# Performance work log

Hardware: AMD Instinct MI355X
Metric: run time of the kernel (lower is better)

## Reference

```python
import jax, jax.numpy as jnp
import numpy as np
import math

D, H = 128, 8
B, LC, LQ = 8, 512, 64


def pos_signal(channels, length):
    # tensor2tensor timing signal, returned as [C, L]
    pos = jnp.arange(length, dtype=jnp.float32)
    nts = channels // 2
    inc = math.log(1.0e4) / (nts - 1)
    inv = jnp.exp(jnp.arange(nts, dtype=jnp.float32) * -inc)
    st = pos[:, None] * inv[None, :]                      # [L, nts]
    sig = jnp.concatenate([jnp.sin(st), jnp.cos(st)], 1)  # [L, C]
    return sig.T


def mask_logits(t, m):
    return t * m + (1.0 - m) * -1e30


def ln_c(x, g, b):  # LayerNorm over channel dim of [B, D, L]
    mu = jnp.mean(x, axis=1, keepdims=True)
    var = jnp.mean((x - mu) ** 2, axis=1, keepdims=True)
    return (x - mu) / jnp.sqrt(var + 1e-5) * g[None, :, None] + b[None, :, None]


def conv1x1(x, w, b=None):  # x [B, I, L], w [O, I]
    y = jnp.einsum('oi,bil->bol', w, x)
    return y if b is None else y + b[None, :, None]


def dw_sep_conv(x, dw, pw, pwb):  # depthwise (k, no bias) -> pointwise (bias) -> relu
    k = dw.shape[-1]
    y = jax.lax.conv_general_dilated(x, dw[:, None, :], (1,), [(k // 2, k // 2)],
        dimension_numbers=('NCH', 'OIH', 'NCH'), feature_group_count=x.shape[1])
    return jax.nn.relu(conv1x1(y, pw, pwb))


def self_attention(x, mem_w, q_w, mask, n_head):  # x [B, D, L]
    b, d, L = x.shape
    dh = d // n_head
    mem = jnp.einsum('oi,bil->blo', mem_w, x)  # [B, L, 2D]
    q = jnp.einsum('oi,bil->blo', q_w, x)      # [B, L, D]
    def heads(t):
        return t.reshape(b, L, n_head, dh).transpose(0, 2, 1, 3)  # [B, H, L, dh]
    Qh = heads(q) * dh ** -0.5
    K = heads(mem[..., :d])
    V = heads(mem[..., d:])
    logits = jnp.einsum('bhqe,bhke->bhqk', Qh, K)
    logits = mask_logits(logits, mask[:, None, None, :])
    w = jax.nn.softmax(logits, axis=-1)
    o = jnp.einsum('bhqk,bhke->bhqe', w, V)
    return o.transpose(0, 2, 1, 3).reshape(b, L, d).transpose(0, 2, 1)


def encoder_block(x, mask, p, n_head):
    out = x + pos_signal(x.shape[1], x.shape[2])[None]
    n_conv = p['dw'].shape[0]
    for i in range(n_conv):
        res = out
        out = ln_c(out, p['lnc_g'][i], p['lnc_b'][i])
        out = dw_sep_conv(out, p['dw'][i], p['pw'][i], p['pw_b'][i]) + res
    res = out
    out = ln_c(out, p['ln1_g'], p['ln1_b'])
    out = self_attention(out, p['mem_w'], p['q_w'], mask, n_head) + res
    res = out
    out = ln_c(out, p['ln2_g'], p['ln2_b'])
    out = jax.nn.relu(conv1x1(out, p['ffn1_w'], p['ffn1_b']))
    out = conv1x1(out, p['ffn2_w'], p['ffn2_b'])
    return out + res


def cq_attention(Ce, Qe, cmask, qmask, w4C, w4Q, w4mlu, cq_b):
    Cx = Ce.transpose(0, 2, 1)   # [B, Lc, 2D]
    Qx = Qe.transpose(0, 2, 1)   # [B, Lq, 2D]
    s0 = jnp.einsum('bld,d->bl', Cx, w4C)[:, :, None]
    s1 = jnp.einsum('bqd,d->bq', Qx, w4Q)[:, None, :]
    s2 = jnp.einsum('bld,bqd->blq', Cx * w4mlu[None, None, :], Qx)
    S = s0 + s1 + s2 + cq_b
    S1 = jax.nn.softmax(mask_logits(S, qmask[:, None, :]), axis=2)
    S2 = jax.nn.softmax(mask_logits(S, cmask[:, :, None]), axis=1)
    A = jnp.einsum('blq,bqd->bld', S1, Qx)
    Bt = jnp.einsum('blq,bmq,bmd->bld', S1, S2, Cx)  # (S1 @ S2^T) @ C
    out = jnp.concatenate([Cx, A, Cx * A, Cx * Bt], axis=2)
    return out.transpose(0, 2, 1)  # [B, 8D, Lc]


def _forward(C, Q, maskC, maskQ, e_dw, e_pw, e_pw_b, e_lnc_g, e_lnc_b, e_mem_w, e_q_w,
             e_ffn1_w, e_ffn1_b, e_ffn2_w, e_ffn2_b, e_ln1_g, e_ln1_b, e_ln2_g, e_ln2_b,
             w4C, w4Q, w4mlu, cq_b, resizer_w,
             m_dw, m_pw, m_pw_b, m_lnc_g, m_lnc_b, m_mem_w, m_q_w,
             m_ffn1_w, m_ffn1_b, m_ffn2_w, m_ffn2_b, m_ln1_g, m_ln1_b, m_ln2_g, m_ln2_b):
    ep = dict(dw=e_dw, pw=e_pw, pw_b=e_pw_b, lnc_g=e_lnc_g, lnc_b=e_lnc_b,
              mem_w=e_mem_w, q_w=e_q_w, ffn1_w=e_ffn1_w, ffn1_b=e_ffn1_b,
              ffn2_w=e_ffn2_w, ffn2_b=e_ffn2_b, ln1_g=e_ln1_g, ln1_b=e_ln1_b,
              ln2_g=e_ln2_g, ln2_b=e_ln2_b)
    mp = dict(dw=m_dw, pw=m_pw, pw_b=m_pw_b, lnc_g=m_lnc_g, lnc_b=m_lnc_b,
              mem_w=m_mem_w, q_w=m_q_w, ffn1_w=m_ffn1_w, ffn1_b=m_ffn1_b,
              ffn2_w=m_ffn2_w, ffn2_b=m_ffn2_b, ln1_g=m_ln1_g, ln1_b=m_ln1_b,
              ln2_g=m_ln2_g, ln2_b=m_ln2_b)
    Ce = encoder_block(C, maskC, ep, H)
    Qe = encoder_block(Q, maskQ, ep, H)
    Ce = jnp.concatenate([Ce, C], axis=1)  # encode_fusion -> [B, 2D, Lc]
    Qe = jnp.concatenate([Qe, Q], axis=1)
    X = cq_attention(Ce, Qe, maskC, maskQ, w4C, w4Q, w4mlu, cq_b)
    X = jnp.concatenate([X, Ce], axis=1)   # match_fusion -> [B, 10D, Lc]
    M0 = conv1x1(X, resizer_w)             # [B, D, Lc]

    def run(m):
        def step(carry, p):
            return encoder_block(carry, maskC, p, H), None
        m, _ = jax.lax.scan(step, m, mp)
        return m

    M1 = run(M0)
    M2 = run(M1)
    M3 = run(M2)
    return M1, M2, M3


def setup_inputs() -> dict:
    key = jax.random.key(0)
    ks = iter(jax.random.split(key, 48))
    def rn(shape, scale):
        return jax.random.normal(next(ks), shape, dtype=jnp.float32) * scale
    s1 = 1.0 / math.sqrt(D)
    s2 = 1.0 / math.sqrt(2 * D)
    f32 = jnp.float32
    return dict(
        C=rn((B, D, LC), 1.0), Q=rn((B, D, LQ), 1.0),
        maskC=jnp.ones((B, LC), f32), maskQ=jnp.ones((B, LQ), f32),
        e_dw=rn((4, D, 7), 1.0 / math.sqrt(7)), e_pw=rn((4, D, D), s1),
        e_pw_b=jnp.zeros((4, D), f32), e_lnc_g=jnp.ones((4, D), f32), e_lnc_b=jnp.zeros((4, D), f32),
        e_mem_w=rn((2 * D, D), s1), e_q_w=rn((D, D), s1),
        e_ffn1_w=rn((D, D), s1), e_ffn1_b=jnp.zeros((D,), f32),
        e_ffn2_w=rn((D, D), s1), e_ffn2_b=jnp.zeros((D,), f32),
        e_ln1_g=jnp.ones((D,), f32), e_ln1_b=jnp.zeros((D,), f32),
        e_ln2_g=jnp.ones((D,), f32), e_ln2_b=jnp.zeros((D,), f32),
        w4C=rn((2 * D,), s2), w4Q=rn((2 * D,), s2), w4mlu=rn((2 * D,), s2),
        cq_b=jnp.zeros((1,), f32),
        resizer_w=rn((D, 10 * D), 1.0 / math.sqrt(10 * D)),
        m_dw=rn((7, 2, D, 5), 1.0 / math.sqrt(5)), m_pw=rn((7, 2, D, D), s1),
        m_pw_b=jnp.zeros((7, 2, D), f32), m_lnc_g=jnp.ones((7, 2, D), f32), m_lnc_b=jnp.zeros((7, 2, D), f32),
        m_mem_w=rn((7, 2 * D, D), s1), m_q_w=rn((7, D, D), s1),
        m_ffn1_w=rn((7, D, D), s1), m_ffn1_b=jnp.zeros((7, D), f32),
        m_ffn2_w=rn((7, D, D), s1), m_ffn2_b=jnp.zeros((7, D), f32),
        m_ln1_g=jnp.ones((7, D), f32), m_ln1_b=jnp.zeros((7, D), f32),
        m_ln2_g=jnp.ones((7, D), f32), m_ln2_b=jnp.zeros((7, D), f32),
    )


def reference(C, Q, maskC, maskQ, e_dw, e_pw, e_pw_b, e_lnc_g, e_lnc_b, e_mem_w, e_q_w,
              e_ffn1_w, e_ffn1_b, e_ffn2_w, e_ffn2_b, e_ln1_g, e_ln1_b, e_ln2_g, e_ln2_b,
              w4C, w4Q, w4mlu, cq_b, resizer_w,
              m_dw, m_pw, m_pw_b, m_lnc_g, m_lnc_b, m_mem_w, m_q_w,
              m_ffn1_w, m_ffn1_b, m_ffn2_w, m_ffn2_b, m_ln1_g, m_ln1_b, m_ln2_g, m_ln2_b):
    return _forward(C, Q, maskC, maskQ, e_dw, e_pw, e_pw_b, e_lnc_g, e_lnc_b, e_mem_w, e_q_w,
                    e_ffn1_w, e_ffn1_b, e_ffn2_w, e_ffn2_b, e_ln1_g, e_ln1_b, e_ln2_g, e_ln2_b,
                    w4C, w4Q, w4mlu, cq_b, resizer_w,
                    m_dw, m_pw, m_pw_b, m_lnc_g, m_lnc_b, m_mem_w, m_q_w,
                    m_ffn1_w, m_ffn1_b, m_ffn2_w, m_ffn2_b, m_ln1_g, m_ln1_b, m_ln2_g, m_ln2_b)
```

## Files before the change

kernel.cpp:

```cpp
#include <hip/hip_runtime.h>
#include <math.h>

#define D_  128
#define B_  8
#define H_  8
#define LC_ 512
#define LQ_ 64

typedef float f32x4 __attribute__((ext_vector_type(4)));
typedef short bf16x8 __attribute__((ext_vector_type(8)));
typedef short short4v __attribute__((ext_vector_type(4)));
typedef unsigned short ushortT;

__device__ inline short bfr(float x) {
  unsigned u = __float_as_uint(x);
  u += 0x7fff + ((u >> 16) & 1);
  return (short)(u >> 16);
}
__device__ inline float bfi(ushortT u) {
  return __uint_as_float(((unsigned)u) << 16);
}

__device__ inline bf16x8 mk8(short4v lo, short4v hi) {
  bf16x8 r;
  r[0] = lo[0]; r[1] = lo[1]; r[2] = lo[2]; r[3] = lo[3];
  r[4] = hi[0]; r[5] = hi[1]; r[6] = hi[2]; r[7] = hi[3];
  return r;
}

__device__ inline bf16x8 ldA(const ushortT* row, int koff) {
  short4v lo = *(const short4v*)(row + koff);
  short4v hi = *(const short4v*)(row + koff + 16);
  return mk8(lo, hi);
}
__device__ inline bf16x8 ldB2(const ushortT* plo, const ushortT* phi) {
  short4v lo = *(const short4v*)plo;
  short4v hi = *(const short4v*)phi;
  return mk8(lo, hi);
}

__global__ void k_prep(const float* a0, const float* a1, const float* a2,
                       const float* a3, const float* a4, const float* a5,
                       const float* a6, const float* a7, const float* a8,
                       const float* a9, const float* a10, ushortT* dst) {
  int i = blockIdx.x * 256 + threadIdx.x;
  if (i >= 1114112) return;
  const float* s; int lo;
  if      (i <   65536) { s = a0;  lo = i; }
  else if (i <   98304) { s = a1;  lo = i - 65536; }
  else if (i <  114688) { s = a2;  lo = i - 98304; }
  else if (i <  131072) { s = a3;  lo = i - 114688; }
  else if (i <  147456) { s = a4;  lo = i - 131072; }
  else if (i <  311296) { s = a5;  lo = i - 147456; }
  else if (i <  540672) { s = a6;  lo = i - 311296; }
  else if (i <  770048) { s = a7;  lo = i - 540672; }
  else if (i <  884736) { s = a8;  lo = i - 770048; }
  else if (i <  999424) { s = a9;  lo = i - 884736; }
  else                  { s = a10; lo = i - 999424; }
  dst[i] = (ushortT)bfr(s[lo]);
}

__global__ void k_postab(float* pos) {
  int i = blockIdx.x * 256 + threadIdx.x;
  int d = i >> 9, l = i & 511;
  int j = d & 63;
  float arg = (float)l * expf(-(float)j * 0.14619588f);
  pos[i] = (d < 64) ? sinf(arg) : cosf(arg);
}

template <int KK, int ADDPOS>
__global__ __launch_bounds__(256) void k_fusedconv(
    const float* __restrict__ xC, float* __restrict__ yC,
    const float* __restrict__ xQ, float* __restrict__ yQ,
    const float* __restrict__ pos,
    const float* __restrict__ dw1, const ushortT* __restrict__ pw1,
    const float* __restrict__ pb1, const float* __restrict__ g1,
    const float* __restrict__ be1,
    const float* __restrict__ dw2, const ushortT* __restrict__ pw2,
    const float* __restrict__ pb2, const float* __restrict__ g2w,
    const float* __restrict__ be2, int ntC) {
  const int HALO = KK / 2;
  const int W1 = 32 + 2 * HALO;
  __shared__ __align__(16) float raw[128 * 40];
  __shared__ __align__(16) ushortT l1o[128 * 36];
  __shared__ __align__(16) ushortT xbf1[32 * 32 * 4];
  __shared__ float mu1[40], rs1[40], mu2[32], rs2[32], ps[160], psq[160];
  ushortT* xbf2 = (ushortT*)raw;
  int bx = blockIdx.x;
  const float* x; float* yout; int l0, L;
  if (bx < ntC) { x = xC; yout = yC; l0 = bx * 16; L = LC_; }
  else          { x = xQ; yout = yQ; l0 = (bx - ntC) * 16; L = LQ_; }
  int o0 = blockIdx.y * 64;
  int b = blockIdx.z;
  int tid = threadIdx.x;
  for (int idx = tid; idx < 128 * W1; idx += 256) {
    int d = idx / W1, c = idx - d * W1;
    int gl = l0 - 8 - HALO + c;
    float v = 0.f;
    if (gl >= 0 && gl < L) {
      v = x[((size_t)b * 128 + d) * L + gl];
      if (ADDPOS) v += pos[d * 512 + gl];
    }
    raw[d * 40 + c] = v;
  }
  __syncthreads();
  if (tid < 4 * W1) {
    int c = tid % W1, hh = tid / W1;
    float s = 0.f, s2 = 0.f;
    for (int d = hh * 32; d < hh * 32 + 32; d++) {
      float v = raw[d * 40 + c];
      s += v; s2 += v * v;
    }
    ps[tid] = s; psq[tid] = s2;
  }
  __syncthreads();
  if (tid < W1) {
    float s = ps[tid] + ps[tid + W1] + ps[tid + 2 * W1] + ps[tid + 3 * W1];
    float s2 = psq[tid] + psq[tid + W1] + psq[tid + 2 * W1] + psq[tid + 3 * W1];
    float mu = s * (1.f / 128.f);
    float var = fmaxf(s2 * (1.f / 128.f) - mu * mu, 0.f);
    mu1[tid] = mu; rs1[tid] = rsqrtf(var + 1e-5f);
  }
  __syncthreads();
  {
    int cc0 = tid & 31, dbase = tid >> 5;
#pragma unroll
    for (int kq = 0; kq < 4; kq++) {
      short4v pk;
#pragma unroll
      for (int e = 0; e < 4; e++) {
        int d = dbase * 16 + kq * 4 + e;
        float gg = g1[d], bb = be1[d];
        const float* wr = dw1 + d * KK;
        float acc = 0.f;
#pragma unroll
        for (int t = 0; t < KK; t++) {
          int ci = cc0 + t;
          int gl = l0 - 8 - HALO + ci;
          float lv = 0.f;
          if (gl >= 0 && gl < L)
            lv = (raw[d * 40 + ci] - mu1[ci]) * rs1[ci] * gg + bb;
          acc += wr[t] * lv;
        }
        pk[e] = bfr(acc);
      }
      *(short4v*)&xbf1[(((dbase * 4 + kq) * 32) + cc0) * 4] = pk;
    }
  }
  __syncthreads();
  int w = tid >> 6, lane = tid & 63, g2 = lane >> 4, r = lane & 15;
  {
    f32x4 acc[2][2];
#pragma unroll
    for (int i = 0; i < 2; i++)
#pragma unroll
      for (int nt = 0; nt < 2; nt++) acc[i][nt] = (f32x4){0.f, 0.f, 0.f, 0.f};
#pragma unroll
    for (int i = 0; i < 2; i++) {
      const ushortT* arow = pw1 + (size_t)((2 * w + i) * 16 + r) * 128;
#pragma unroll
      for (int kk = 0; kk < 4; kk++) {
        bf16x8 a = ldA(arow, kk * 32 + g2 * 4);
#pragma unroll
        for (int nt = 0; nt < 2; nt++) {
          bf16x8 bb = ldB2(&xbf1[(((kk * 8 + g2) * 32) + nt * 16 + r) * 4],
                           &xbf1[(((kk * 8 + 4 + g2) * 32) + nt * 16 + r) * 4]);
          acc[i][nt] = __builtin_amdgcn_mfma_f32_16x16x32_bf16(a, bb, acc[i][nt], 0, 0, 0);
        }
      }
    }
#pragma unroll
    for (int i = 0; i < 2; i++)
#pragma unroll
      for (int nt = 0; nt < 2; nt++)
#pragma unroll
        for (int p = 0; p < 4; p++) {
          int o = (2 * w + i) * 16 + g2 * 4 + p;
          int c1 = nt * 16 + r;
          int gl = l0 - 8 + c1;
          float val = 0.f;
          if (gl >= 0 && gl < L)
            val = fmaxf(acc[i][nt][p] + pb1[o], 0.f) + raw[o * 40 + c1 + HALO];
          l1o[o * 36 + c1] = (ushortT)bfr(val);
        }
  }
  __syncthreads();
  if (tid < 128) {
    int c = tid & 31, hh = tid >> 5;
    float s = 0.f, s2 = 0.f;
    for (int d = hh * 32; d < hh * 32 + 32; d++) {
      float v = bfi(l1o[d * 36 + c]);
      s += v; s2 += v * v;
    }
    ps[tid] = s; psq[tid] = s2;
  }
  __syncthreads();
  if (tid < 32) {
    float s = ps[tid] + ps[tid + 32] + ps[tid + 64] + ps[tid + 96];
    float s2 = psq[tid] + psq[tid + 32] + psq[tid + 64] + psq[tid + 96];
    float mu = s * (1.f / 128.f);
    float var = fmaxf(s2 * (1.f / 128.f) - mu * mu, 0.f);
    mu2[tid] = mu; rs2[tid] = rsqrtf(var + 1e-5f);
  }
  __syncthreads();
  {
    int cc2 = tid & 15, db2 = tid >> 4;
#pragma unroll
    for (int kq = 0; kq < 2; kq++) {
      short4v pk;
#pragma unroll
      for (int e = 0; e < 4; e++) {
        int d = db2 * 8 + kq * 4 + e;
        float gg = g2w[d], bb = be2[d];
        const float* wr = dw2 + d * KK;
        float acc = 0.f;
#pragma unroll
        for (int t = 0; t < KK; t++) {
          int c1 = cc2 + 8 + t - HALO;
          int gl = l0 + cc2 + t - HALO;
          float lv = 0.f;
          if (gl >= 0 && gl < L)
            lv = (bfi(l1o[d * 36 + c1]) - mu2[c1]) * rs2[c1] * gg + bb;
          acc += wr[t] * lv;
        }
        pk[e] = bfr(acc);
      }
      *(short4v*)&xbf2[(((db2 * 2 + kq) * 16) + cc2) * 4] = pk;
    }
  }
  __syncthreads();
  {
    f32x4 a2 = {0.f, 0.f, 0.f, 0.f};
    const ushortT* arow = pw2 + (size_t)(o0 + 16 * w + r) * 128;
#pragma unroll
    for (int kk = 0; kk < 4; kk++) {
      bf16x8 a = ldA(arow, kk * 32 + g2 * 4);
      bf16x8 bb = ldB2(&xbf2[(((kk * 8 + g2) * 16) + r) * 4],
                       &xbf2[(((kk * 8 + 4 + g2) * 16) + r) * 4]);
      a2 = __builtin_amdgcn_mfma_f32_16x16x32_bf16(a, bb, a2, 0, 0, 0);
    }
#pragma unroll
    for (int p = 0; p < 4; p++) {
      int o = o0 + 16 * w + g2 * 4 + p;
      yout[((size_t)b * 128 + o) * L + l0 + r] =
          fmaxf(a2[p] + pb2[o], 0.f) + bfi(l1o[o * 36 + 8 + r]);
    }
  }
}

template <int KK, int ADDPOS>
__global__ __launch_bounds__(1024) void k_convproj1024(
    const float* __restrict__ xC, float* __restrict__ yC,
    ushortT* __restrict__ mkvC, ushortT* __restrict__ qpC,
    const float* __restrict__ xQ, float* __restrict__ yQ,
    ushortT* __restrict__ mkvQ, ushortT* __restrict__ qpQ,
    const float* __restrict__ pos,
    const float* __restrict__ dw1, const ushortT* __restrict__ pw1,
    const float* __restrict__ pb1, const float* __restrict__ g1,
    const float* __restrict__ be1,
    const float* __restrict__ dw2, const ushortT* __restrict__ pw2,
    const float* __restrict__ pb2, const float* __restrict__ g2w,
    const float* __restrict__ be2,
    const ushortT* __restrict__ memw, const ushortT* __restrict__ qw,
    const float* __restrict__ g3, const float* __restrict__ be3, int ntC) {
  const int HALO = KK / 2;
  const int W1 = 32 + 2 * HALO;
  __shared__ __align__(16) float raw[128 * 40];
  __shared__ __align__(16) ushortT l1o[128 * 36];
  __shared__ __align__(16) ushortT xbf1[32 * 32 * 4];
  __shared__ __align__(16) ushortT c2o[128 * 16];
  __shared__ float mu1[40], rs1[40], mu2[32], rs2[32], mu3[16], rs3[16];
  __shared__ float ps[160], psq[160];
  ushortT* xbf2 = (ushortT*)raw;
  ushortT* xbf3 = (ushortT*)(raw + 4096);
  int bx = blockIdx.x;
  const float* x; float* yout; ushortT* mkv; ushortT* qp; int l0, L;
  if (bx < ntC) { x = xC; yout = yC; mkv = mkvC; qp = qpC; l0 = bx * 16; L = LC_; }
  else          { x = xQ; yout = yQ; mkv = mkvQ; qp = qpQ; l0 = (bx - ntC) * 16; L = LQ_; }
  int b = blockIdx.z;
  int tid = threadIdx.x;
  for (int idx = tid; idx < 128 * W1; idx += 1024) {
    int d = idx / W1, c = idx - d * W1;
    int gl = l0 - 8 - HALO + c;
    float v = 0.f;
    if (gl >= 0 && gl < L) {
      v = x[((size_t)b * 128 + d) * L + gl];
      if (ADDPOS) v += pos[d * 512 + gl];
    }
    raw[d * 40 + c] = v;
  }
  __syncthreads();
  if (tid < 4 * W1) {
    int c = tid % W1, hh = tid / W1;
    float s = 0.f, s2 = 0.f;
    for (int d = hh * 32; d < hh * 32 + 32; d++) {
      float v = raw[d * 40 + c];
      s += v; s2 += v * v;
    }
    ps[tid] = s; psq[tid] = s2;
  }
  __syncthreads();
  if (tid < W1) {
    float s = ps[tid] + ps[tid + W1] + ps[tid + 2 * W1] + ps[tid + 3 * W1];
    float s2 = psq[tid] + psq[tid + W1] + psq[tid + 2 * W1] + psq[tid + 3 * W1];
    float mu = s * (1.f / 128.f);
    float var = fmaxf(s2 * (1.f / 128.f) - mu * mu, 0.f);
    mu1[tid] = mu; rs1[tid] = rsqrtf(var + 1e-5f);
  }
  __syncthreads();
  {
    int cc0 = tid & 31, dbase = tid >> 5;
    short4v pk;
#pragma unroll
    for (int e = 0; e < 4; e++) {
      int d = dbase * 4 + e;
      float gg = g1[d], bb = be1[d];
      const float* wr = dw1 + d * KK;
      float acc = 0.f;
#pragma unroll
      for (int t = 0; t < KK; t++) {
        int ci = cc0 + t;
        int gl = l0 - 8 - HALO + ci;
        float lv = 0.f;
        if (gl >= 0 && gl < L)
          lv = (raw[d * 40 + ci] - mu1[ci]) * rs1[ci] * gg + bb;
        acc += wr[t] * lv;
      }
      pk[e] = bfr(acc);
    }
    *(short4v*)&xbf1[((dbase * 32) + cc0) * 4] = pk;
  }
  __syncthreads();
  int w = tid >> 6, lane = tid & 63, g2 = lane >> 4, r = lane & 15;
  {
    int m = w & 7, nt = w >> 3;
    f32x4 acc = {0.f, 0.f, 0.f, 0.f};
    const ushortT* arow = pw1 + (size_t)(m * 16 + r) * 128;
#pragma unroll
    for (int kk = 0; kk < 4; kk++) {
      bf16x8 a = ldA(arow, kk * 32 + g2 * 4);
      bf16x8 bb = ldB2(&xbf1[(((kk * 8 + g2) * 32) + nt * 16 + r) * 4],
                       &xbf1[(((kk * 8 + 4 + g2) * 32) + nt * 16 + r) * 4]);
      acc = __builtin_amdgcn_mfma_f32_16x16x32_bf16(a, bb, acc, 0, 0, 0);
    }
#pragma unroll
    for (int p = 0; p < 4; p++) {
      int o = m * 16 + g2 * 4 + p;
      int c1 = nt * 16 + r;
      int gl = l0 - 8 + c1;
      float val = 0.f;
      if (gl >= 0 && gl < L)
        val = fmaxf(acc[p] + pb1[o], 0.f) + raw[o * 40 + c1 + HALO];
      l1o[o * 36 + c1] = (ushortT)bfr(val);
    }
  }
  __syncthreads();
  if (tid < 128) {
    int c = tid & 31, hh = tid >> 5;
    float s = 0.f, s2 = 0.f;
    for (int d = hh * 32; d < hh * 32 + 32; d++) {
      float v = bfi(l1o[d * 36 + c]);
      s += v; s2 += v * v;
    }
    ps[tid] = s; psq[tid] = s2;
  }
  __syncthreads();
  if (tid < 32) {
    float s = ps[tid] + ps[tid + 32] + ps[tid + 64] + ps[tid + 96];
    float s2 = psq[tid] + psq[tid + 32] + psq[tid + 64] + psq[tid + 96];
    float mu = s * (1.f / 128.f);
    float var = fmaxf(s2 * (1.f / 128.f) - mu * mu, 0.f);
    mu2[tid] = mu; rs2[tid] = rsqrtf(var + 1e-5f);
  }
  __syncthreads();
  {
    int cc2 = tid & 15, db2 = tid >> 4;
#pragma unroll
    for (int e = 0; e < 2; e++) {
      int d = db2 * 2 + e;
      float gg = g2w[d], bb = be2[d];
      const float* wr = dw2 + d * KK;
      float acc = 0.f;
#pragma unroll
      for (int t = 0; t < KK; t++) {
        int c1 = cc2 + 8 + t - HALO;
        int gl = l0 + cc2 + t - HALO;
        float lv = 0.f;
        if (gl >= 0 && gl < L)
          lv = (bfi(l1o[d * 36 + c1]) - mu2[c1]) * rs2[c1] * gg + bb;
        acc += wr[t] * lv;
      }
      xbf2[(((d >> 2) * 16) + cc2) * 4 + (d & 3)] = (ushortT)bfr(acc);
    }
  }
  __syncthreads();
  if (w < 8) {
    f32x4 a2 = {0.f, 0.f, 0.f, 0.f};
    const ushortT* arow = pw2 + (size_t)(w * 16 + r) * 128;
#pragma unroll
    for (int kk = 0; kk < 4; kk++) {
      bf16x8 a = ldA(arow, kk * 32 + g2 * 4);
      bf16x8 bb = ldB2(&xbf2[(((kk * 8 + g2) * 16) + r) * 4],
                       &xbf2[(((kk * 8 + 4 + g2) * 16) + r) * 4]);
      a2 = __builtin_amdgcn_mfma_f32_16x16x32_bf16(a, bb, a2, 0, 0, 0);
    }
#pragma unroll
    for (int p = 0; p < 4; p++) {
      int o = w * 16 + g2 * 4 + p;
      float val = fmaxf(a2[p] + pb2[o], 0.f) + bfi(l1o[o * 36 + 8 + r]);
      yout[((size_t)b * 128 + o) * L + l0 + r] = val;
      c2o[o * 16 + r] = (ushortT)bfr(val);
    }
  }
  __syncthreads();
  if (tid < 128) {
    int c = tid & 15, hh = tid >> 4;
    float s = 0.f, s2 = 0.f;
    for (int d = hh * 16; d < hh * 16 + 16; d++) {
      float v = bfi(c2o[d * 16 + c]);
      s += v; s2 += v * v;
    }
    ps[tid] = s; psq[tid] = s2;
  }
  __syncthreads();
  if (tid < 16) {
    float s = 0.f, s2 = 0.f;
#pragma unroll
    for (int hh = 0; hh < 8; hh++) { s += ps[hh * 16 + tid]; s2 += psq[hh * 16 + tid]; }
    float mu = s * (1.f / 128.f);
    float var = fmaxf(s2 * (1.f / 128.f) - mu * mu, 0.f);
    mu3[tid] = mu; rs3[tid] = rsqrtf(var + 1e-5f);
  }
  __syncthreads();
  for (int idx = tid; idx < 2048; idx += 1024) {
    int d = idx >> 4, c = idx & 15;
    float val = (bfi(c2o[d * 16 + c]) - mu3[c]) * rs3[c] * g3[d] + be3[d];
    xbf3[(((d >> 2) * 16) + c) * 4 + (d & 3)] = (ushortT)bfr(val);
  }
  __syncthreads();
#pragma unroll
  for (int t = 0; t < 2; t++) {
    int mt = w + 16 * t;
    if (mt < 24) {
      const ushortT* arow; ushortT* outp; int obase, O;
      if (mt < 16) { arow = memw + (size_t)(mt * 16 + r) * 128; outp = mkv; obase = mt * 16; O = 256; }
      else         { arow = qw + (size_t)((mt - 16) * 16 + r) * 128; outp = qp; obase = (mt - 16) * 16; O = 128; }
      f32x4 acc = {0.f, 0.f, 0.f, 0.f};
#pragma unroll
      for (int kk = 0; kk < 4; kk++) {
        bf16x8 a = ldA(arow, kk * 32 + g2 * 4);
        bf16x8 bb = ldB2(&xbf3[(((kk * 8 + g2) * 16) + r) * 4],
                         &xbf3[(((kk * 8 + 4 + g2) * 16) + r) * 4]);
        acc = __builtin_amdgcn_mfma_f32_16x16x32_bf16(a, bb, acc, 0, 0, 0);
      }
#pragma unroll
      for (int p = 0; p < 4; p++)
        outp[((size_t)b * O + obase + g2 * 4 + p) * L + l0 + r] = (ushortT)bfr(acc[p]);
    }
  }
}

template <int NCH, int WOUT>
__device__ __forceinline__ void attn_body(
    char* smem, const ushortT* memKV, const ushortT* qp, const float* mask,
    float* cur, const ushortT* w1bf, const float* b1,
    const ushortT* w2bf, const float* b2,
    const float* g, const float* be, float* wout, int q0, int b, int L, int tid) {
  float* msh = (float*)smem;
  float* ssh = (float*)(smem + 2048);
  float* OshF = (float*)(smem + 4096);
  float* updT = (float*)(smem + 12288);
  ushortT* xbf = (ushortT*)(smem + 20480);
  ushortT* midbf = (ushortT*)(smem + 24576);
  float* mu_s = (float*)(smem + 28672);
  float* rs_s = (float*)(smem + 28736);
  float* ps = (float*)(smem + 28800);
  float* psq = (float*)(smem + 32896);
  int w = tid >> 6;
  int h = w & 7, kh = w >> 3;
  int lane = tid & 63;
  int g2 = lane >> 4, r = lane & 15;
  const ushortT* qb = qp + ((size_t)b * 128 + h * 16) * L;
  const ushortT* kb = memKV + ((size_t)b * 256 + h * 16) * L;
  const ushortT* vb = memKV + ((size_t)b * 256 + 128 + h * 16) * L;
  const float* mk = mask + (size_t)b * L;
  int qcol = q0 + r;
  bf16x8 qf;
#pragma unroll
  for (int j = 0; j < 4; j++)
    qf[j] = bfr(bfi(qb[(size_t)(g2 * 4 + j) * L + qcol]) * 0.25f);
  qf[4] = 0; qf[5] = 0; qf[6] = 0; qf[7] = 0;
  float m_run = -INFINITY, ssum = 0.f;
  f32x4 O = {0.f, 0.f, 0.f, 0.f};
  int kbeg = kh * (L / 2), kend = (kh + 1) * (L / 2);
  for (int k0 = kbeg; k0 < kend; k0 += NCH * 16) {
    f32x4 sd[NCH];
#pragma unroll
    for (int mc = 0; mc < NCH; mc++) {
      bf16x8 kf;
      int krow = k0 + mc * 16 + r;
#pragma unroll
      for (int j = 0; j < 4; j++)
        kf[j] = (short)kb[(size_t)(g2 * 4 + j) * L + krow];
      kf[4] = 0; kf[5] = 0; kf[6] = 0; kf[7] = 0;
      f32x4 z = {0.f, 0.f, 0.f, 0.f};
      sd[mc] = __builtin_amdgcn_mfma_f32_16x16x32_bf16(kf, qf, z, 0, 0, 0);
    }
    float tm = -INFINITY;
#pragma unroll
    for (int mc = 0; mc < NCH; mc++) {
#pragma unroll
      for (int p = 0; p < 4; p++) {
        float mv = mk[k0 + mc * 16 + g2 * 4 + p];
        float sv = sd[mc][p] * mv + (1.f - mv) * (-1e30f);
        sd[mc][p] = sv;
        tm = fmaxf(tm, sv);
      }
    }
    tm = fmaxf(tm, __shfl_xor(tm, 16));
    tm = fmaxf(tm, __shfl_xor(tm, 32));
    float nm = fmaxf(m_run, tm);
    float c = __expf(m_run - nm);
    ssum *= c;
    O[0] *= c; O[1] *= c; O[2] *= c; O[3] *= c;
    float psum = 0.f;
    bf16x8 pf[NCH / 2];
#pragma unroll
    for (int c2 = 0; c2 < NCH / 2; c2++) {
#pragma unroll
      for (int j = 0; j < 4; j++) {
        float e0 = __expf(sd[2 * c2][j] - nm);
        float e1 = __expf(sd[2 * c2 + 1][j] - nm);
        psum += e0 + e1;
        pf[c2][j] = bfr(e0);
        pf[c2][j + 4] = bfr(e1);
      }
    }
    psum += __shfl_xor(psum, 16);
    psum += __shfl_xor(psum, 32);
    ssum += psum;
#pragma unroll
    for (int c2 = 0; c2 < NCH / 2; c2++) {
      const ushortT* vrow = vb + (size_t)r * L + k0 + c2 * 32 + g2 * 4;
      short4v lo = *(const short4v*)vrow;
      short4v hi = *(const short4v*)(vrow + 16);
      bf16x8 vf = mk8(lo, hi);
      O = __builtin_amdgcn_mfma_f32_16x16x32_bf16(vf, pf[c2], O, 0, 0, 0);
    }
    m_run = nm;
  }
  if (kh == 1) {
    msh[h * 64 + lane] = m_run;
    ssh[h * 64 + lane] = ssum;
#pragma unroll
    for (int p = 0; p < 4; p++) OshF[(h * 64 + lane) * 4 + p] = O[p];
  }
  __syncthreads();
  if (kh == 0) {
    float mB = msh[h * 64 + lane], sB = ssh[h * 64 + lane];
    float nm = fmaxf(m_run, mB);
    float cA = __expf(m_run - nm), cB = __expf(mB - nm);
    float inv = 1.f / (ssum * cA + sB * cB);
#pragma unroll
    for (int p = 0; p < 4; p++) {
      int d = h * 16 + g2 * 4 + p;
      float ov = (O[p] * cA + OshF[(h * 64 + lane) * 4 + p] * cB) * inv;
      updT[d * 16 + r] = cur[((size_t)b * 128 + d) * L + qcol] + ov;
    }
  }
  __syncthreads();
  {
    int c = tid & 15, hh = tid >> 4;
    float s = 0.f, s2 = 0.f;
    for (int d = hh * 2; d < hh * 2 + 2; d++) {
      float v = updT[d * 16 + c];
      s += v; s2 += v * v;
    }
    ps[tid] = s; psq[tid] = s2;
  }
  __syncthreads();
  if (tid < 16) {
    float s = 0.f, s2 = 0.f;
    for (int hh = 0; hh < 64; hh++) { s += ps[hh * 16 + tid]; s2 += psq[hh * 16 + tid]; }
    float mu = s * (1.f / 128.f);
    float var = fmaxf(s2 * (1.f / 128.f) - mu * mu, 0.f);
    mu_s[tid] = mu; rs_s[tid] = rsqrtf(var + 1e-5f);
  }
  __syncthreads();
  for (int idx = tid; idx < 2048; idx += 1024) {
    int d = idx >> 4, c = idx & 15;
    float val = (updT[d * 16 + c] - mu_s[c]) * rs_s[c] * g[d] + be[d];
    xbf[(((d >> 2) * 16) + c) * 4 + (d & 3)] = (ushortT)bfr(val);
  }
  __syncthreads();
  int w8 = tid >> 6;
  int g2b = (tid & 63) >> 4, rb = tid & 15;
  if (w8 < 8) {
    f32x4 acc = {0.f, 0.f, 0.f, 0.f};
    const ushortT* ar = w1bf + (size_t)(16 * w8 + rb) * 128;
#pragma unroll
    for (int kk = 0; kk < 4; kk++) {
      bf16x8 a = ldA(ar, kk * 32 + g2b * 4);
      bf16x8 bb = ldB2(&xbf[(((kk * 8 + g2b) * 16) + rb) * 4],
                       &xbf[(((kk * 8 + 4 + g2b) * 16) + rb) * 4]);
      acc = __builtin_amdgcn_mfma_f32_16x16x32_bf16(a, bb, acc, 0, 0, 0);
    }
#pragma unroll
    for (int p = 0; p < 4; p++) {
      int dmid = 16 * w8 + g2b * 4 + p;
      float val = fmaxf(acc[p] + b1[dmid], 0.f);
      midbf[(((4 * w8 + g2b) * 16) + rb) * 4 + p] = (ushortT)bfr(val);
    }
  }
  __syncthreads();
  if (w8 < 8) {
    f32x4 a2 = {0.f, 0.f, 0.f, 0.f};
    const ushortT* ar = w2bf + (size_t)(16 * w8 + rb) * 128;
#pragma unroll
    for (int kk = 0; kk < 4; kk++) {
      bf16x8 a = ldA(ar, kk * 32 + g2b * 4);
      bf16x8 bb = ldB2(&midbf[(((kk * 8 + g2b) * 16) + rb) * 4],
                       &midbf[(((kk * 8 + 4 + g2b) * 16) + rb) * 4]);
      a2 = __builtin_amdgcn_mfma_f32_16x16x32_bf16(a, bb, a2, 0, 0, 0);
    }
#pragma unroll
    for (int p = 0; p < 4; p++) {
      int o = 16 * w8 + g2b * 4 + p;
      size_t pos2 = ((size_t)b * 128 + o) * L + q0 + rb;
      float val = a2[p] + b2[o] + updT[o * 16 + rb];
      cur[pos2] = val;
      if (WOUT) wout[pos2] = val;
    }
  }
}

template <int WOUT>
__global__ __launch_bounds__(1024) void k_attnffn_m(
    const ushortT* memKV, const ushortT* qp, const float* mask, float* cur,
    const ushortT* w1bf, const float* b1, const ushortT* w2bf, const float* b2,
    const float* g, const float* be, float* wout) {
  __shared__ __align__(16) char smem[36992];
  attn_body<8, WOUT>(smem, memKV, qp, mask, cur, w1bf, b1, w2bf, b2, g, be,
                     wout, blockIdx.x * 16, blockIdx.z, LC_, threadIdx.x);
}

__global__ __launch_bounds__(1024) void k_attnffn_in(
    const ushortT* mkvC, const ushortT* qpC, const float* maskC, float* curC,
    const ushortT* mkvQ, const ushortT* qpQ, const float* maskQ, float* curQ,
    const ushortT* w1bf, const float* b1, const ushortT* w2bf, const float* b2,
    const float* g, const float* be, int ntC) {
  __shared__ __align__(16) char smem[36992];
  int bx = blockIdx.x;
  if (bx < ntC)
    attn_body<8, 0>(smem, mkvC, qpC, maskC, curC, w1bf, b1, w2bf, b2, g, be,
                    nullptr, bx * 16, blockIdx.z, LC_, threadIdx.x);
  else
    attn_body<2, 0>(smem, mkvQ, qpQ, maskQ, curQ, w1bf, b1, w2bf, b2, g, be,
                    nullptr, (bx - ntC) * 16, blockIdx.z, LQ_, threadIdx.x);
}


__global__ void k_concat2m(const float* __restrict__ x1C, const float* __restrict__ x2C,
                           float* __restrict__ outC,
                           const float* __restrict__ x1Q, const float* __restrict__ x2Q,
                           float* __restrict__ outQ) {
  int idx = blockIdx.x * 256 + threadIdx.x;
  const int tot1 = B_ * 256 * LC_;
  const int tot2 = B_ * 256 * LQ_;
  if (idx < tot1) {
    int l = idx % LC_;
    int c = (idx / LC_) & 255;
    int b = idx / (LC_ * 256);
    float v = (c < 128) ? x1C[((size_t)b * 128 + c) * LC_ + l]
                        : x2C[((size_t)b * 128 + (c - 128)) * LC_ + l];
    outC[idx] = v;
  } else {
    int i2 = idx - tot1;
    if (i2 < tot2) {
      int l = i2 % LQ_;
      int c = (i2 / LQ_) & 255;
      int b = i2 / (LQ_ * 256);
      float v = (c < 128) ? x1Q[((size_t)b * 128 + c) * LQ_ + l]
                          : x2Q[((size_t)b * 128 + (c - 128)) * LQ_ + l];
      outQ[i2] = v;
    }
  }
}

__global__ void k_cqSrow(const float* __restrict__ Ce, const float* __restrict__ Qe,
                         const float* __restrict__ w4C, const float* __restrict__ w4Q,
                         const float* __restrict__ w4mlu, const float* __restrict__ cqb,
                         const float* __restrict__ qmask,
                         float* __restrict__ S, float* __restrict__ S1) {
  int idx = blockIdx.x * 256 + threadIdx.x;
  int q = idx & 63;
  int l = (idx >> 6) % LC_;
  int b = (idx >> 6) / LC_;
  const float* ce = Ce + (size_t)b * 256 * LC_ + l;
  const float* qe = Qe + (size_t)b * 256 * LQ_ + q;
  float acc = 0.f, a0 = 0.f, a1 = 0.f;
#pragma unroll 8
  for (int j = 0; j < 256; j++) {
    float cv = ce[(size_t)j * LC_];
    float qv = qe[(size_t)j * LQ_];
    acc += cv * w4mlu[j] * qv;
    a0 += cv * w4C[j];
    a1 += qv * w4Q[j];
  }
  float sv = acc + a0 + a1 + cqb[0];
  S[idx] = sv;
  float mv = qmask[b * LQ_ + q];
  float v = sv * mv + (1.f - mv) * (-1e30f);
  float mx = v;
  for (int off = 32; off; off >>= 1) mx = fmaxf(mx, __shfl_xor(mx, off));
  float p = expf(v - mx);
  float s = p;
  for (int off = 32; off; off >>= 1) s += __shfl_xor(s, off);
  S1[idx] = p / s;
}

__global__ __launch_bounds__(256) void k_softmax_col(
    const float* __restrict__ S, const float* __restrict__ cmask, float* __restrict__ S2) {
  int q = blockIdx.x & 63, b = blockIdx.x >> 6;
  int tid = threadIdx.x;
  __shared__ float redm[4], reds[4];
  const float* col = S + (size_t)b * LC_ * LQ_ + q;
  const float* mk = cmask + b * LC_;
  float vm[2];
#pragma unroll
  for (int k = 0; k < 2; k++) {
    int l = tid + 256 * k;
    float mv = mk[l];
    vm[k] = col[(size_t)l * LQ_] * mv + (1.f - mv) * (-1e30f);
  }
  float mx = fmaxf(vm[0], vm[1]);
  for (int off = 32; off; off >>= 1) mx = fmaxf(mx, __shfl_xor(mx, off));
  if ((tid & 63) == 0) redm[tid >> 6] = mx;
  __syncthreads();
  mx = fmaxf(fmaxf(redm[0], redm[1]), fmaxf(redm[2], redm[3]));
  float e0 = expf(vm[0] - mx), e1 = expf(vm[1] - mx);
  float s = e0 + e1;
  for (int off = 32; off; off >>= 1) s += __shfl_xor(s, off);
  if ((tid & 63) == 0) reds[tid >> 6] = s;
  __syncthreads();
  float invs = 1.f / (reds[0] + reds[1] + reds[2] + reds[3]);
  float* out = S2 + (size_t)b * LC_ * LQ_ + q;
  out[(size_t)tid * LQ_] = e0 * invs;
  out[(size_t)(tid + 256) * LQ_] = e1 * invs;
}

__global__ void k_cqY(const float* __restrict__ S2, const float* __restrict__ Ce,
                      float* __restrict__ Y) {
  int idx = blockIdx.x * 256 + threadIdx.x;
  if (idx >= B_ * 256 * LQ_) return;
  int q = idx & 63;
  int j = (idx >> 6) & 255;
  int b = idx >> 14;
  const float* s2 = S2 + (size_t)b * LC_ * LQ_ + q;
  const float* ce = Ce + ((size_t)b * 256 + j) * LC_;
  float acc = 0.f;
#pragma unroll 8
  for (int l = 0; l < LC_; l++) acc += s2[(size_t)l * LQ_] * ce[l];
  Y[idx] = acc;
}

__global__ __launch_bounds__(256) void k_cqAB(
    const float* __restrict__ S1, const float* __restrict__ Qe, const float* __restrict__ Y,
    float* __restrict__ A, float* __restrict__ Bt) {
  __shared__ float s1s[64][65];
  int l0 = blockIdx.x * 64;
  int b = blockIdx.z;
  int tid = threadIdx.x;
  for (int idx = tid; idx < 64 * 64; idx += 256) {
    int l = idx >> 6, q = idx & 63;
    s1s[l][q] = S1[((size_t)b * LC_ + l0 + l) * LQ_ + q];
  }
  __syncthreads();
  int ll = tid & 63, jj = tid >> 6;
  int j = blockIdx.y * 4 + jj;
  const float* qe = Qe + ((size_t)b * 256 + j) * LQ_;
  const float* yb = Y + ((size_t)b * 256 + j) * LQ_;
  float a = 0.f, bt = 0.f;
#pragma unroll 8
  for (int q = 0; q < 64; q++) {
    float sv = s1s[ll][q];
    a += sv * qe[q];
    bt += sv * yb[q];
  }
  A[((size_t)b * 256 + j) * LC_ + l0 + ll] = a;
  Bt[((size_t)b * 256 + j) * LC_ + l0 + ll] = bt;
}

__global__ __launch_bounds__(512) void k_resizer512(
    const float* __restrict__ Ce, const float* __restrict__ A,
    const float* __restrict__ Bt, const ushortT* __restrict__ wbf,
    float* __restrict__ y) {
  __shared__ __align__(16) ushortT xbf[32 * 16 * 4];
  int l0 = blockIdx.x * 16;
  int b = blockIdx.z;
  int tid = threadIdx.x;
  int w = tid >> 6, lane = tid & 63, g2 = lane >> 4, r = lane & 15;
  const ushortT* arow = wbf + (size_t)(16 * w + r) * 1280;
  f32x4 acc = {0.f, 0.f, 0.f, 0.f};
  for (int kt = 0; kt < 1280; kt += 128) {
    __syncthreads();
    for (int idx = tid; idx < 2048; idx += 512) {
      int kl = idx >> 4, cc = idx & 15;
      int ch = kt + kl;
      int seg = ch >> 8;
      int j = ch & 255;
      size_t p = ((size_t)b * 256 + j) * LC_ + l0 + cc;
      float v;
      if (seg == 0 || seg == 4) v = Ce[p];
      else if (seg == 1) v = A[p];
      else if (seg == 2) v = Ce[p] * A[p];
      else v = Ce[p] * Bt[p];
      xbf[((kl >> 2) * 16 + cc) * 4 + (kl & 3)] = (ushortT)bfr(v);
    }
    __syncthreads();
#pragma unroll
    for (int kk2 = 0; kk2 < 4; kk2++) {
      bf16x8 a = ldA(arow, kt + kk2 * 32 + g2 * 4);
      bf16x8 b0 = ldB2(&xbf[(((kk2 * 8 + g2) * 16) + r) * 4],
                       &xbf[(((kk2 * 8 + 4 + g2) * 16) + r) * 4]);
      acc = __builtin_amdgcn_mfma_f32_16x16x32_bf16(a, b0, acc, 0, 0, 0);
    }
  }
#pragma unroll
  for (int p = 0; p < 4; p++) {
    int o = 16 * w + g2 * 4 + p;
    y[((size_t)b * D_ + o) * LC_ + l0 + r] = acc[p];
  }
}


extern "C" void kernel_launch(void* const* d_in, const int* in_sizes, int n_in,
                              void* d_out, int out_size, void* d_ws, size_t ws_size,
                              hipStream_t stream) {
  (void)in_sizes; (void)n_in; (void)out_size; (void)ws_size;
  const float* C        = (const float*)d_in[0];
  const float* Q        = (const float*)d_in[1];
  const float* maskC    = (const float*)d_in[2];
  const float* maskQ    = (const float*)d_in[3];
  const float* e_dw     = (const float*)d_in[4];
  const float* e_pw     = (const float*)d_in[5];
  const float* e_pw_b   = (const float*)d_in[6];
  const float* e_lnc_g  = (const float*)d_in[7];
  const float* e_lnc_b  = (const float*)d_in[8];
  const float* e_mem_w  = (const float*)d_in[9];
  const float* e_q_w    = (const float*)d_in[10];
  const float* e_ffn1_w = (const float*)d_in[11];
  const float* e_ffn1_b = (const float*)d_in[12];
  const float* e_ffn2_w = (const float*)d_in[13];
  const float* e_ffn2_b = (const float*)d_in[14];
  const float* e_ln1_g  = (const float*)d_in[15];
  const float* e_ln1_b  = (const float*)d_in[16];
  const float* e_ln2_g  = (const float*)d_in[17];
  const float* e_ln2_b  = (const float*)d_in[18];
  const float* w4C      = (const float*)d_in[19];
  const float* w4Q      = (const float*)d_in[20];
  const float* w4mlu    = (const float*)d_in[21];
  const float* cq_b     = (const float*)d_in[22];
  const float* resizer_w= (const float*)d_in[23];
  const float* m_dw     = (const float*)d_in[24];
  const float* m_pw     = (const float*)d_in[25];
  const float* m_pw_b   = (const float*)d_in[26];
  const float* m_lnc_g  = (const float*)d_in[27];
  const float* m_lnc_b  = (const float*)d_in[28];
  const float* m_mem_w  = (const float*)d_in[29];
  const float* m_q_w    = (const float*)d_in[30];
  const float* m_ffn1_w = (const float*)d_in[31];
  const float* m_ffn1_b = (const float*)d_in[32];
  const float* m_ffn2_w = (const float*)d_in[33];
  const float* m_ffn2_b = (const float*)d_in[34];
  const float* m_ln1_g  = (const float*)d_in[35];
  const float* m_ln1_b  = (const float*)d_in[36];
  const float* m_ln2_g  = (const float*)d_in[37];
  const float* m_ln2_b  = (const float*)d_in[38];

  float* ws = (float*)d_ws;
  const size_t SB = (size_t)B_ * D_ * LC_;
  float* cur  = ws;
  float* aux  = cur + SB;
  float* mkvF = aux + SB;
  float* qpbF = mkvF + 2 * SB;
  float* Ce   = qpbF + SB;
  float* Qe   = Ce + 2 * SB;
  float* Sbuf = Qe + (size_t)B_ * 256 * LQ_;
  float* S1   = Sbuf + (size_t)B_ * LC_ * LQ_;
  float* S2   = S1 + (size_t)B_ * LC_ * LQ_;
  float* Yb   = S2 + (size_t)B_ * LC_ * LQ_;
  float* Mb   = Yb + (size_t)B_ * 256 * LQ_;
  float* Ab   = mkvF;
  float* Bb   = cur;
  ushortT* mkvB = (ushortT*)mkvF;
  ushortT* qpbB = (ushortT*)qpbF;
  ushortT* wb = (ushortT*)(Mb + SB);
  ushortT* w_epw  = wb;
  ushortT* w_emem = wb + 65536;
  ushortT* w_eq   = wb + 98304;
  ushortT* w_ef1  = wb + 114688;
  ushortT* w_ef2  = wb + 131072;
  ushortT* w_rsz  = wb + 147456;
  ushortT* w_mpw  = wb + 311296;
  ushortT* w_mmem = wb + 540672;
  ushortT* w_mq   = wb + 770048;
  ushortT* w_mf1  = wb + 884736;
  ushortT* w_mf2  = wb + 999424;
  float* after_wb = (float*)(wb + 1114112);
  float* curQ  = after_wb;
  float* auxQ  = curQ + 65536;
  ushortT* mkvQB = (ushortT*)(auxQ + 65536);
  ushortT* qpbQB = (ushortT*)(auxQ + 131072);
  float* posT  = auxQ + 196608;

  k_prep<<<(1114112 + 255) / 256, 256, 0, stream>>>(
      e_pw, e_mem_w, e_q_w, e_ffn1_w, e_ffn2_w, resizer_w,
      m_pw, m_mem_w, m_q_w, m_ffn1_w, m_ffn2_w, wb);
  k_postab<<<256, 256, 0, stream>>>(posT);

  k_fusedconv<7, 1><<<dim3(36, 2, B_), 256, 0, stream>>>(
      C, cur, Q, curQ, posT,
      e_dw + 0 * 896, w_epw + 0, e_pw_b + 0, e_lnc_g + 0, e_lnc_b + 0,
      e_dw + 1 * 896, w_epw + 16384, e_pw_b + 128, e_lnc_g + 128, e_lnc_b + 128, 32);
  k_convproj1024<7, 0><<<dim3(36, 1, B_), 1024, 0, stream>>>(
      cur, aux, mkvB, qpbB, curQ, auxQ, mkvQB, qpbQB, posT,
      e_dw + 2 * 896, w_epw + 32768, e_pw_b + 256, e_lnc_g + 256, e_lnc_b + 256,
      e_dw + 3 * 896, w_epw + 49152, e_pw_b + 384, e_lnc_g + 384, e_lnc_b + 384,
      w_emem, w_eq, e_ln1_g, e_ln1_b, 32);
  k_attnffn_in<<<dim3(36, 1, B_), 1024, 0, stream>>>(
      mkvB, qpbB, maskC, aux, mkvQB, qpbQB, maskQ, auxQ,
      w_ef1, e_ffn1_b, w_ef2, e_ffn2_b, e_ln2_g, e_ln2_b, 32);
  k_concat2m<<<(B_ * 256 * (LC_ + LQ_) + 255) / 256, 256, 0, stream>>>(
      aux, C, Ce, auxQ, Q, Qe);

  k_cqSrow<<<(B_ * LC_ * LQ_) / 256, 256, 0, stream>>>(Ce, Qe, w4C, w4Q, w4mlu, cq_b, maskQ, Sbuf, S1);
  k_softmax_col<<<B_ * LQ_, 256, 0, stream>>>(Sbuf, maskC, S2);
  k_cqY<<<(B_ * 256 * LQ_) / 256, 256, 0, stream>>>(S2, Ce, Yb);
  k_cqAB<<<dim3(LC_ / 64, 64, B_), 256, 0, stream>>>(S1, Qe, Yb, Ab, Bb);
  k_resizer512<<<dim3(LC_ / 16, 1, B_), 512, 0, stream>>>(Ce, Ab, Bb, w_rsz, Mb);

  float* out = (float*)d_out;
  float* bufs[2] = {cur, aux};
  int cb = 0;
  const float* src = Mb;
  for (int r = 0; r < 3; r++) {
    for (int bi = 0; bi < 7; bi++) {
      int pc0 = bi * 2, pc1 = bi * 2 + 1;
      float* ob = bufs[cb];
      k_convproj1024<5, 1><<<dim3(32, 1, B_), 1024, 0, stream>>>(
          src, ob, mkvB, qpbB, src, ob, mkvB, qpbB, posT,
          m_dw + (size_t)pc0 * 640, w_mpw + (size_t)pc0 * 16384, m_pw_b + pc0 * 128,
          m_lnc_g + pc0 * 128, m_lnc_b + pc0 * 128,
          m_dw + (size_t)pc1 * 640, w_mpw + (size_t)pc1 * 16384, m_pw_b + pc1 * 128,
          m_lnc_g + pc1 * 128, m_lnc_b + pc1 * 128,
          w_mmem + (size_t)bi * 32768, w_mq + (size_t)bi * 16384,
          m_ln1_g + bi * 128, m_ln1_b + bi * 128, 32);
      if (bi == 6)
        k_attnffn_m<1><<<dim3(32, 1, B_), 1024, 0, stream>>>(
            mkvB, qpbB, maskC, ob,
            w_mf1 + (size_t)bi * 16384, m_ffn1_b + bi * 128,
            w_mf2 + (size_t)bi * 16384, m_ffn2_b + bi * 128,
            m_ln2_g + bi * 128, m_ln2_b + bi * 128, out + (size_t)r * SB);
      else
        k_attnffn_m<0><<<dim3(32, 1, B_), 1024, 0, stream>>>(
            mkvB, qpbB, maskC, ob,
            w_mf1 + (size_t)bi * 16384, m_ffn1_b + bi * 128,
            w_mf2 + (size_t)bi * 16384, m_ffn2_b + bi * 128,
            m_ln2_g + bi * 128, m_ln2_b + bi * 128, nullptr);
      src = ob;
      cb ^= 1;
    }
  }
}
```

Before: 1.241 ms.

## Split fused conv+projection kernel into separate conv and LN+QKV projection kernels

Measured after the change: 1.517 ms. +22.2%, slower.

```diff
diff --git a/kernel.cpp b/kernel.cpp
--- a/kernel.cpp
+++ b/kernel.cpp
@@ -245,6 +245,66 @@
       yout[((size_t)b * 128 + o) * L + l0 + r] =
           fmaxf(a2[p] + pb2[o], 0.f) + bfi(l1o[o * 36 + 8 + r]);
     }
+  }
+}
+
+__global__ __launch_bounds__(512) void k_proj(
+    const float* __restrict__ x, const ushortT* __restrict__ memw,
+    const ushortT* __restrict__ qw, const float* __restrict__ g3,
+    const float* __restrict__ be3, ushortT* __restrict__ mkv,
+    ushortT* __restrict__ qp) {
+  __shared__ float xs[128 * 16];
+  __shared__ __align__(16) ushortT xbf3[128 * 16];
+  __shared__ float mu_s[16], rs_s[16], ps[512], psq[512];
+  int l0 = blockIdx.x * 16;
+  int b = blockIdx.z;
+  int tid = threadIdx.x;
+  {
+    int c = tid & 15, hh = tid >> 4;
+    float s = 0.f, s2 = 0.f;
+#pragma unroll
+    for (int e = 0; e < 4; e++) {
+      int d = hh * 4 + e;
+      float v = x[((size_t)b * 128 + d) * LC_ + l0 + c];
+      xs[d * 16 + c] = v;
+      s += v; s2 += v * v;
+    }
+    ps[tid] = s; psq[tid] = s2;
+  }
+  __syncthreads();
+  if (tid < 16) {
+    float s = 0.f, s2 = 0.f;
+#pragma unroll
+    for (int hh = 0; hh < 32; hh++) { s += ps[hh * 16 + tid]; s2 += psq[hh * 16 + tid]; }
+    float mu = s * (1.f / 128.f);
+    float var = fmaxf(s2 * (1.f / 128.f) - mu * mu, 0.f);
+    mu_s[tid] = mu; rs_s[tid] = rsqrtf(var + 1e-5f);
+  }
+  __syncthreads();
+  for (int idx = tid; idx < 2048; idx += 512) {
+    int d = idx >> 4, c = idx & 15;
+    float val = (xs[d * 16 + c] - mu_s[c]) * rs_s[c] * g3[d] + be3[d];
+    xbf3[(((d >> 2) * 16) + c) * 4 + (d & 3)] = (ushortT)bfr(val);
+  }
+  __syncthreads();
+  int w = tid >> 6, lane = tid & 63, g2 = lane >> 4, r = lane & 15;
+#pragma unroll
+  for (int t = 0; t < 3; t++) {
+    int mt = w + 8 * t;
+    const ushortT* arow; ushortT* outp; int obase, O;
+    if (mt < 16) { arow = memw + (size_t)(mt * 16 + r) * 128; outp = mkv; obase = mt * 16; O = 256; }
+    else         { arow = qw + (size_t)((mt - 16) * 16 + r) * 128; outp = qp; obase = (mt - 16) * 16; O = 128; }
+    f32x4 acc = {0.f, 0.f, 0.f, 0.f};
+#pragma unroll
+    for (int kk = 0; kk < 4; kk++) {
+      bf16x8 a = ldA(arow, kk * 32 + g2 * 4);
+      bf16x8 bb = ldB2(&xbf3[(((kk * 8 + g2) * 16) + r) * 4],
+                       &xbf3[(((kk * 8 + 4 + g2) * 16) + r) * 4]);
+      acc = __builtin_amdgcn_mfma_f32_16x16x32_bf16(a, bb, acc, 0, 0, 0);
+    }
+#pragma unroll
+    for (int p = 0; p < 4; p++)
+      outp[((size_t)b * O + obase + g2 * 4 + p) * LC_ + l0 + r] = (ushortT)bfr(acc[p]);
   }
 }
 
@@ -948,14 +1008,15 @@
     for (int bi = 0; bi < 7; bi++) {
       int pc0 = bi * 2, pc1 = bi * 2 + 1;
       float* ob = bufs[cb];
-      k_convproj1024<5, 1><<<dim3(32, 1, B_), 1024, 0, stream>>>(
-          src, ob, mkvB, qpbB, src, ob, mkvB, qpbB, posT,
+      k_fusedconv<5, 1><<<dim3(32, 2, B_), 256, 0, stream>>>(
+          src, ob, src, ob, posT,
           m_dw + (size_t)pc0 * 640, w_mpw + (size_t)pc0 * 16384, m_pw_b + pc0 * 128,
           m_lnc_g + pc0 * 128, m_lnc_b + pc0 * 128,
           m_dw + (size_t)pc1 * 640, w_mpw + (size_t)pc1 * 16384, m_pw_b + pc1 * 128,
-          m_lnc_g + pc1 * 128, m_lnc_b + pc1 * 128,
-          w_mmem + (size_t)bi * 32768, w_mq + (size_t)bi * 16384,
-          m_ln1_g + bi * 128, m_ln1_b + bi * 128, 32);
+          m_lnc_g + pc1 * 128, m_lnc_b + pc1 * 128, 32);
+      k_proj<<<dim3(32, 1, B_), 512, 0, stream>>>(
+          ob, w_mmem + (size_t)bi * 32768, w_mq + (size_t)bi * 16384,
+          m_ln1_g + bi * 128, m_ln1_b + bi * 128, mkvB, qpbB);
       if (bi == 6)
         k_attnffn_m<1><<<dim3(32, 1, B_), 1024, 0, stream>>>(
             mkvB, qpbB, maskC, ob,
```
